# Optimization experiments

Hardware: AMD Instinct MI355X
Metric: run time of the kernel (lower is better)

The kernel has to match this reference:

```python
import jax, jax.numpy as jnp
import numpy as np
import math

B, DG, P, DA = 512, 1024, 1024, 256
LN_EPS = 1e-5  # torch LayerNorm default
EPS = 1e-12


def _ln(x, g, b):
    mu = jnp.mean(x, axis=-1, keepdims=True)
    var = jnp.mean((x - mu) ** 2, axis=-1, keepdims=True)
    return (x - mu) * jax.lax.rsqrt(var + LN_EPS) * g + b


def setup_inputs() -> dict:
    key = jax.random.key(0)
    ks = jax.random.split(key, 16)
    s = lambda fan_in: 1.0 / math.sqrt(fan_in)
    return {
        "hg": jax.random.normal(ks[0], (B, DG), jnp.float32),
        "desc_2d": jax.random.normal(ks[1], (B, P), jnp.float32),
        "Wq": jax.random.uniform(ks[2], (DA, DG), jnp.float32, -s(DG), s(DG)),
        "bq": jnp.zeros((DA,), jnp.float32),
        "wk_val": jax.random.uniform(ks[3], (DA,), jnp.float32, -1.0, 1.0),
        "bk_val": jax.random.uniform(ks[4], (DA,), jnp.float32, -1.0, 1.0),
        "wv_val": jax.random.uniform(ks[5], (DA,), jnp.float32, -1.0, 1.0),
        "bv_val": jax.random.uniform(ks[6], (DA,), jnp.float32, -1.0, 1.0),
        "Ek": jax.random.normal(ks[7], (P, DA), jnp.float32),
        "Ev": jax.random.normal(ks[8], (P, DA), jnp.float32),
        "Uq": jax.random.uniform(ks[9], (DA, DA), jnp.float32, -s(DA), s(DA)),
        "Vk": jax.random.uniform(ks[10], (DA, DA), jnp.float32, -s(DA), s(DA)),
        "ln_q_g": jnp.ones((DA,), jnp.float32), "ln_q_b": jnp.zeros((DA,), jnp.float32),
        "ln_k_g": jnp.ones((DA,), jnp.float32), "ln_k_b": jnp.zeros((DA,), jnp.float32),
        "ln_v_g": jnp.ones((DA,), jnp.float32), "ln_v_b": jnp.zeros((DA,), jnp.float32),
    }


def reference(hg, desc_2d, Wq, bq, wk_val, bk_val, wv_val, bv_val, Ek, Ev, Uq, Vk,
              ln_q_g, ln_q_b, ln_k_g, ln_k_b, ln_v_g, ln_v_b):
    # dropout is inference-mode (identity)
    q = _ln(hg @ Wq.T + bq, ln_q_g, ln_q_b)                       # (B, DA)
    # scalar -> token proj plus id embedding
    k = desc_2d[:, :, None] * wk_val + bk_val + Ek[None]          # (B, P, DA)
    v = desc_2d[:, :, None] * wv_val + bv_val + Ev[None]
    k = _ln(k, ln_k_g, ln_k_b)
    v = _ln(v, ln_v_g, ln_v_b)
    q2 = q @ Uq.T                                                 # (B, DA)
    k2 = jnp.einsum('bpd,ed->bpe', k, Vk)                         # (B, P, DA)
    e = jnp.einsum('bpd,bd->bp', k2, q2) / math.sqrt(DA)          # (B, P)
    alpha = jax.nn.sigmoid(e)
    alpha = alpha / (jnp.sum(alpha, axis=1, keepdims=True) + EPS)
    c = jnp.einsum('bp,bpd->bd', alpha, v)                        # (B, DA)
    return c, alpha
```

## Files before the change

### kernel.cpp

```cpp
#include <hip/hip_runtime.h>
#include <math.h>

#define B 512
#define DG 1024
#define P 1024
#define DA 256
#define LDP 68

__device__ __forceinline__ float block_reduce_sum(float v, volatile float* red) {
    #pragma unroll
    for (int off = 32; off > 0; off >>= 1) v += __shfl_down(v, off, 64);
    const int lane = threadIdx.x & 63, wid = threadIdx.x >> 6;
    __syncthreads();
    if (lane == 0) red[wid] = v;
    __syncthreads();
    return red[0] + red[1] + red[2] + red[3];
}

#define FMA16(a4, b4, acc)                                   \
    acc[0][0] = fmaf(a4.x, b4.x, acc[0][0]);                 \
    acc[0][1] = fmaf(a4.x, b4.y, acc[0][1]);                 \
    acc[0][2] = fmaf(a4.x, b4.z, acc[0][2]);                 \
    acc[0][3] = fmaf(a4.x, b4.w, acc[0][3]);                 \
    acc[1][0] = fmaf(a4.y, b4.x, acc[1][0]);                 \
    acc[1][1] = fmaf(a4.y, b4.y, acc[1][1]);                 \
    acc[1][2] = fmaf(a4.y, b4.z, acc[1][2]);                 \
    acc[1][3] = fmaf(a4.y, b4.w, acc[1][3]);                 \
    acc[2][0] = fmaf(a4.z, b4.x, acc[2][0]);                 \
    acc[2][1] = fmaf(a4.z, b4.y, acc[2][1]);                 \
    acc[2][2] = fmaf(a4.z, b4.z, acc[2][2]);                 \
    acc[2][3] = fmaf(a4.z, b4.w, acc[2][3]);                 \
    acc[3][0] = fmaf(a4.w, b4.x, acc[3][0]);                 \
    acc[3][1] = fmaf(a4.w, b4.y, acc[3][1]);                 \
    acc[3][2] = fmaf(a4.w, b4.z, acc[3][2]);                 \
    acc[3][3] = fmaf(a4.w, b4.w, acc[3][3]);

__global__ __launch_bounds__(256) void KA(const float* __restrict__ hg, const float* __restrict__ Wq,
                                          const float* __restrict__ Uq,
                                          const float* __restrict__ Ek, const float* __restrict__ Ev,
                                          const float* __restrict__ wk, const float* __restrict__ bk,
                                          const float* __restrict__ wv, const float* __restrict__ bv,
                                          float* __restrict__ qp, float* __restrict__ UqT,
                                          float* __restrict__ pst, float* __restrict__ scal4) {
    __shared__ __align__(16) float sA[32 * LDP];
    __shared__ __align__(16) float sB[32 * LDP];
    __shared__ float red[4];
    const int tid = threadIdx.x;
    const int bi = blockIdx.x;

    if (bi < 256) {
        const int mt = bi & 7, nt = (bi >> 3) & 3, ks = bi >> 5;
        const int b0 = mt * 64, d0 = nt * 64, kc = ks * 128;
        const int sm = tid >> 3, sk4 = (tid & 7) * 4;
        const int ty4 = (tid >> 4) * 4, tx4 = (tid & 15) * 4;
        float acc[4][4] = {};
        for (int kt = 0; kt < 128; kt += 32) {
            const int kg = kc + kt;
            #pragma unroll
            for (int pass = 0; pass < 2; ++pass) {
                int m = sm + pass * 32;
                float4 av = *reinterpret_cast<const float4*>(&hg[(b0 + m) * DG + kg + sk4]);
                sA[(sk4 + 0) * LDP + m] = av.x; sA[(sk4 + 1) * LDP + m] = av.y;
                sA[(sk4 + 2) * LDP + m] = av.z; sA[(sk4 + 3) * LDP + m] = av.w;
                float4 wv4 = *reinterpret_cast<const float4*>(&Wq[(d0 + m) * DG + kg + sk4]);
                sB[(sk4 + 0) * LDP + m] = wv4.x; sB[(sk4 + 1) * LDP + m] = wv4.y;
                sB[(sk4 + 2) * LDP + m] = wv4.z; sB[(sk4 + 3) * LDP + m] = wv4.w;
            }
            __syncthreads();
            #pragma unroll
            for (int kk = 0; kk < 32; ++kk) {
                float4 a4 = *reinterpret_cast<const float4*>(&sA[kk * LDP + ty4]);
                float4 b4 = *reinterpret_cast<const float4*>(&sB[kk * LDP + tx4]);
                FMA16(a4, b4, acc)
            }
            __syncthreads();
        }
        float* outp = qp + ks * (B * DA);
        #pragma unroll
        for (int i = 0; i < 4; ++i) {
            float4 o = make_float4(acc[i][0], acc[i][1], acc[i][2], acc[i][3]);
            *reinterpret_cast<float4*>(&outp[(b0 + ty4 + i) * DA + d0 + tx4]) = o;
        }
    } else if (bi < 320) {
        const int b2 = bi - 256;
        const int e0 = (b2 & 7) * 32, f0 = (b2 >> 3) * 32;
        const int col = tid & 31, row8 = tid >> 5;
        #pragma unroll
        for (int pass = 0; pass < 4; ++pass) {
            int r = row8 + pass * 8;
            sA[r * 33 + col] = Uq[(e0 + r) * DA + f0 + col];
        }
        __syncthreads();
        #pragma unroll
        for (int pass = 0; pass < 4; ++pass) {
            int r = row8 + pass * 8;
            UqT[(f0 + r) * DA + e0 + col] = sA[col * 33 + r];
        }
    } else {
        const int p = bi - 320, d = tid;
        const float inv = 1.0f / DA;
        float ek = Ek[p * DA + d], ev = Ev[p * DA + d];
        float wkd = wk[d], wvd = wv[d];
        float ck = bk[d] + ek, cv = bv[d] + ev;

        float Sck  = block_reduce_sum(ck, red);
        float Sck2 = block_reduce_sum(ck * ck, red);
        float Swck = block_reduce_sum(wkd * ck, red);
        float Scv  = block_reduce_sum(cv, red);
        float Scv2 = block_reduce_sum(cv * cv, red);
        float Swcv = block_reduce_sum(wvd * cv, red);
        float Swk  = block_reduce_sum(wkd, red);
        float Swv  = block_reduce_sum(wvd, red);

        float mwk = Swk * inv, mwv = Swv * inv;
        float mck = Sck * inv, mcv = Scv * inv;
        if (d == 0) {
            pst[0 * P + p] = mck;
            pst[1 * P + p] = Swck * inv - mwk * mck;
            pst[2 * P + p] = Sck2 * inv - mck * mck;
            pst[3 * P + p] = mcv;
            pst[4 * P + p] = Swcv * inv - mwv * mcv;
            pst[5 * P + p] = Scv2 * inv - mcv * mcv;
        }
        if (p == 0) {
            float Swk2 = block_reduce_sum(wkd * wkd, red);
            float Swv2 = block_reduce_sum(wvd * wvd, red);
            if (d == 0) {
                scal4[0] = mwk;
                scal4[1] = Swk2 * inv - mwk * mwk;
                scal4[2] = mwv;
                scal4[3] = Swv2 * inv - mwv * mwv;
            }
        }
    }
}

__global__ __launch_bounds__(256) void KC(const float* __restrict__ qp, const float* __restrict__ bq,
                                          const float* __restrict__ gq, const float* __restrict__ bqln,
                                          const float* __restrict__ UqT, const float* __restrict__ Vk,
                                          const float* __restrict__ gk,
                                          const float* __restrict__ wk, const float* __restrict__ bk,
                                          const float* __restrict__ bkln,
                                          float* __restrict__ gr, float* __restrict__ bscal) {
    __shared__ __align__(16) float q_lds[DA];
    __shared__ __align__(16) float q2_lds[DA];
    __shared__ float red[4];
    const int b = blockIdx.x, d = threadIdx.x;
    float x = bq[d];
    #pragma unroll
    for (int ks = 0; ks < 8; ++ks) x += qp[ks * (B * DA) + b * DA + d];
    float mu = block_reduce_sum(x, red) * (1.0f / DA);
    float xc = x - mu;
    float var = block_reduce_sum(xc * xc, red) * (1.0f / DA);
    float qv = xc * rsqrtf(var + 1e-5f) * gq[d] + bqln[d];
    q_lds[d] = qv;
    __syncthreads();

    float q2 = 0.f;
    for (int f = 0; f < DA; f += 4) {
        float4 qf = *reinterpret_cast<const float4*>(&q_lds[f]);
        q2 = fmaf(qf.x, UqT[(f + 0) * DA + d], q2);
        q2 = fmaf(qf.y, UqT[(f + 1) * DA + d], q2);
        q2 = fmaf(qf.z, UqT[(f + 2) * DA + d], q2);
        q2 = fmaf(qf.w, UqT[(f + 3) * DA + d], q2);
    }
    q2_lds[d] = q2;
    __syncthreads();

    float r = 0.f;
    for (int e = 0; e < DA; e += 4) {
        float4 qe = *reinterpret_cast<const float4*>(&q2_lds[e]);
        r = fmaf(qe.x, Vk[(e + 0) * DA + d], r);
        r = fmaf(qe.y, Vk[(e + 1) * DA + d], r);
        r = fmaf(qe.z, Vk[(e + 2) * DA + d], r);
        r = fmaf(qe.w, Vk[(e + 3) * DA + d], r);
    }
    float grv = gk[d] * r;
    gr[b * DA + d] = grv;

    float Wg = block_reduce_sum(wk[d] * grv, red);
    float Cg = block_reduce_sum(bk[d] * grv, red);
    float G  = block_reduce_sum(grv, red);
    float Bb = block_reduce_sum(bkln[d] * r, red);
    if (d == 0) {
        bscal[b] = Wg; bscal[B + b] = Cg; bscal[2 * B + b] = G; bscal[3 * B + b] = Bb;
    }
}

__global__ __launch_bounds__(256) void KD(const float* __restrict__ gr, const float* __restrict__ Ek,
                                          float* __restrict__ epart) {
    __shared__ __align__(16) float sA[32 * LDP];
    __shared__ __align__(16) float sB[32 * LDP];
    const int tid = threadIdx.x, bi = blockIdx.x;
    const int mt = bi & 7, nt = (bi >> 3) & 15, ks = bi >> 7;
    const int b0 = mt * 64, p0 = nt * 64, kc = ks * 128;
    const int sm = tid >> 3, sk4 = (tid & 7) * 4;
    const int ty4 = (tid >> 4) * 4, tx4 = (tid & 15) * 4;
    float acc[4][4] = {};
    for (int kt = 0; kt < 128; kt += 32) {
        const int kg = kc + kt;
        #pragma unroll
        for (int pass = 0; pass < 2; ++pass) {
            int m = sm + pass * 32;
            float4 av = *reinterpret_cast<const float4*>(&gr[(b0 + m) * DA + kg + sk4]);
            sA[(sk4 + 0) * LDP + m] = av.x; sA[(sk4 + 1) * LDP + m] = av.y;
            sA[(sk4 + 2) * LDP + m] = av.z; sA[(sk4 + 3) * LDP + m] = av.w;
            float4 ev = *reinterpret_cast<const float4*>(&Ek[(p0 + m) * DA + kg + sk4]);
            sB[(sk4 + 0) * LDP + m] = ev.x; sB[(sk4 + 1) * LDP + m] = ev.y;
            sB[(sk4 + 2) * LDP + m] = ev.z; sB[(sk4 + 3) * LDP + m] = ev.w;
        }
        __syncthreads();
        #pragma unroll
        for (int kk = 0; kk < 32; ++kk) {
            float4 a4 = *reinterpret_cast<const float4*>(&sA[kk * LDP + ty4]);
            float4 b4 = *reinterpret_cast<const float4*>(&sB[kk * LDP + tx4]);
            FMA16(a4, b4, acc)
        }
        __syncthreads();
    }
    float* outp = epart + ks * (B * P);
    #pragma unroll
    for (int i = 0; i < 4; ++i) {
        float4 o = make_float4(acc[i][0], acc[i][1], acc[i][2], acc[i][3]);
        *reinterpret_cast<float4*>(&outp[(b0 + ty4 + i) * P + p0 + tx4]) = o;
    }
}

__global__ __launch_bounds__(256) void KE(const float* __restrict__ epart, const float* __restrict__ desc,
                                          const float* __restrict__ bscal, const float* __restrict__ pst,
                                          const float* __restrict__ scal4,
                                          const float* __restrict__ gv, const float* __restrict__ wv,
                                          const float* __restrict__ bvv, const float* __restrict__ bvln,
                                          float* __restrict__ alpha_out, float* beta,
                                          float* __restrict__ out_c) {
    __shared__ float red[4];
    const int b = blockIdx.x, tid = threadIdx.x;
    const float mwk = scal4[0], Ak = scal4[1], mwv = scal4[2], Av = scal4[3];
    const float Wg = bscal[b], Cg = bscal[B + b], G = bscal[2 * B + b], Bb = bscal[3 * B + b];
    float u[4], sv[4];
    float usum = 0.f;
    #pragma unroll
    for (int j = 0; j < 4; ++j) {
        int p = j * 256 + tid;
        float dot = epart[b * P + p] + epart[B * P + b * P + p];
        float s = desc[b * P + p];
        float mck = pst[p], Bk = pst[P + p], Ck = pst[2 * P + p];
        float var = fmaf(s, fmaf(s, Ak, 2.0f * Bk), Ck);
        float rstd = rsqrtf(var + 1e-5f);
        float mu = fmaf(s, mwk, mck);
        float e = (rstd * (fmaf(s, Wg, Cg) + dot - mu * G) + Bb) * 0.0625f;
        float uu = 1.0f / (1.0f + expf(-e));
        u[j] = uu; sv[j] = s; usum += uu;
    }
    float S = block_reduce_sum(usum, red);
    float invS = 1.0f / (S + 1e-12f);
    float T = S * invS;
    float SB = 0.f, SBs = 0.f, SBm = 0.f;
    #pragma unroll
    for (int j = 0; j < 4; ++j) {
        int p = j * 256 + tid;
        float a = u[j] * invS;
        alpha_out[b * P + p] = a;
        float s = sv[j];
        float mcv = pst[3 * P + p], Bv = pst[4 * P + p], Cv = pst[5 * P + p];
        float var = fmaf(s, fmaf(s, Av, 2.0f * Bv), Cv);
        float rv = rsqrtf(var + 1e-5f);
        float bt = a * rv;
        beta[b * P + p] = bt;
        SB += bt;
        SBs = fmaf(bt, s, SBs);
        SBm = fmaf(bt, fmaf(s, mwv, mcv), SBm);
    }
    SB  = block_reduce_sum(SB, red);
    SBs = block_reduce_sum(SBs, red);
    SBm = block_reduce_sum(SBm, red);
    out_c[b * DA + tid] = gv[tid] * (wv[tid] * SBs + bvv[tid] * SB - SBm) + bvln[tid] * T;
}

__global__ __launch_bounds__(256) void KF(const float* __restrict__ beta, const float* __restrict__ Ev,
                                          float* __restrict__ cpart) {
    __shared__ __align__(16) float sA[32 * LDP];
    __shared__ __align__(16) float sB[32 * LDP];
    const int tid = threadIdx.x, bi = blockIdx.x;
    const int mt = bi & 7, nt = (bi >> 3) & 3, ks = bi >> 5;
    const int b0 = mt * 64, d0 = nt * 64, kc = ks * 128;
    const int sm = tid >> 3, sk4 = (tid & 7) * 4;
    const int kr = tid >> 4, n4 = (tid & 15) * 4;
    const int ty4 = (tid >> 4) * 4, tx4 = (tid & 15) * 4;
    float acc[4][4] = {};
    for (int kt = 0; kt < 128; kt += 32) {
        const int kg = kc + kt;
        #pragma unroll
        for (int pass = 0; pass < 2; ++pass) {
            int m = sm + pass * 32;
            float4 av = *reinterpret_cast<const float4*>(&beta[(b0 + m) * P + kg + sk4]);
            sA[(sk4 + 0) * LDP + m] = av.x; sA[(sk4 + 1) * LDP + m] = av.y;
            sA[(sk4 + 2) * LDP + m] = av.z; sA[(sk4 + 3) * LDP + m] = av.w;
            int k = kr + pass * 16;
            *reinterpret_cast<float4*>(&sB[k * LDP + n4]) =
                *reinterpret_cast<const float4*>(&Ev[(kg + k) * DA + d0 + n4]);
        }
        __syncthreads();
        #pragma unroll
        for (int kk = 0; kk < 32; ++kk) {
            float4 a4 = *reinterpret_cast<const float4*>(&sA[kk * LDP + ty4]);
            float4 b4 = *reinterpret_cast<const float4*>(&sB[kk * LDP + tx4]);
            FMA16(a4, b4, acc)
        }
        __syncthreads();
    }
    float* outp = cpart + ks * (B * DA);
    #pragma unroll
    for (int i = 0; i < 4; ++i) {
        float4 o = make_float4(acc[i][0], acc[i][1], acc[i][2], acc[i][3]);
        *reinterpret_cast<float4*>(&outp[(b0 + ty4 + i) * DA + d0 + tx4]) = o;
    }
}

__global__ __launch_bounds__(256) void KG(const float* __restrict__ cpart, const float* __restrict__ gv,
                                          float* __restrict__ out_c) {
    const int b = blockIdx.x, d = threadIdx.x;
    float s = 0.f;
    #pragma unroll
    for (int ks = 0; ks < 8; ++ks) s += cpart[ks * (B * DA) + b * DA + d];
    out_c[b * DA + d] = fmaf(gv[d], s, out_c[b * DA + d]);
}

extern "C" void kernel_launch(void* const* d_in, const int* in_sizes, int n_in,
                              void* d_out, int out_size, void* d_ws, size_t ws_size,
                              hipStream_t stream) {
    (void)in_sizes; (void)n_in; (void)out_size; (void)ws_size;
    const float* hg   = (const float*)d_in[0];
    const float* desc = (const float*)d_in[1];
    const float* Wq   = (const float*)d_in[2];
    const float* bq   = (const float*)d_in[3];
    const float* wk   = (const float*)d_in[4];
    const float* bk   = (const float*)d_in[5];
    const float* wv   = (const float*)d_in[6];
    const float* bv   = (const float*)d_in[7];
    const float* Ek   = (const float*)d_in[8];
    const float* Ev   = (const float*)d_in[9];
    const float* Uq   = (const float*)d_in[10];
    const float* Vk   = (const float*)d_in[11];
    const float* gq   = (const float*)d_in[12];
    const float* bqln = (const float*)d_in[13];
    const float* gk   = (const float*)d_in[14];
    const float* bkln = (const float*)d_in[15];
    const float* gv   = (const float*)d_in[16];
    const float* bvln = (const float*)d_in[17];

    float* out = (float*)d_out;
    float* out_c = out;
    float* out_alpha = out + B * DA;

    float* ws = (float*)d_ws;
    float* qp    = ws;
    float* epart = ws;
    float* beta  = ws;
    float* gr    = ws + 1048576;
    float* UqT   = ws + 1179648;
    float* cpart = ws + 524288;
    float* bscal = ws + 1572864;
    float* pst   = ws + 1574912;
    float* scal4 = ws + 1581056;

    KA<<<1344, 256, 0, stream>>>(hg, Wq, Uq, Ek, Ev, wk, bk, wv, bv, qp, UqT, pst, scal4);
    KC<<<512, 256, 0, stream>>>(qp, bq, gq, bqln, UqT, Vk, gk, wk, bk, bkln, gr, bscal);
    KD<<<256, 256, 0, stream>>>(gr, Ek, epart);
    KE<<<512, 256, 0, stream>>>(epart, desc, bscal, pst, scal4, gv, wv, bv, bvln, out_alpha, beta, out_c);
    KF<<<256, 256, 0, stream>>>(beta, Ev, cpart);
    KG<<<512, 256, 0, stream>>>(cpart, gv, out_c);
}
```

Measured before the change: 60.74 us.

## Reassociate attention scores via precomputed Uq^T Vk Ek matrix, defer normalization

Instead of computing q2 and gk*Vk^T q2 per batch row and then a B×P×DA GEMM against Ek, the code precomputes a batch-independent matrix N = Uq^T (gk∘Vk) Ek^T (DA×P) in KA/KC. Scores then come from a single q·N GEMM with K=DA that is fused with the sigmoid/LN-stat epilogue in KD, and the per-row scalar reductions come from precomputed vec4 vectors. Alpha normalization is deferred to the final kernel, so the Ev GEMM runs on unnormalized weights and KG rescales by 1/S. This drops one kernel launch and the split-K partials for the scores, but adds two DA×DA×P precompute GEMMs, more cpart splits and more workspace traffic.

After: 66.47 us. 9.4% more time.

```diff
diff --git a/kernel.cpp b/kernel.cpp
--- a/kernel.cpp
+++ b/kernel.cpp
@@ -35,13 +35,25 @@
     acc[3][2] = fmaf(a4.w, b4.z, acc[3][2]);                 \
     acc[3][3] = fmaf(a4.w, b4.w, acc[3][3]);
 
+#define FMA8(a0, a1, b4, acc)                                \
+    acc[0][0] = fmaf(a0, b4.x, acc[0][0]);                   \
+    acc[0][1] = fmaf(a0, b4.y, acc[0][1]);                   \
+    acc[0][2] = fmaf(a0, b4.z, acc[0][2]);                   \
+    acc[0][3] = fmaf(a0, b4.w, acc[0][3]);                   \
+    acc[1][0] = fmaf(a1, b4.x, acc[1][0]);                   \
+    acc[1][1] = fmaf(a1, b4.y, acc[1][1]);                   \
+    acc[1][2] = fmaf(a1, b4.z, acc[1][2]);                   \
+    acc[1][3] = fmaf(a1, b4.w, acc[1][3]);
+
 __global__ __launch_bounds__(256) void KA(const float* __restrict__ hg, const float* __restrict__ Wq,
-                                          const float* __restrict__ Uq,
+                                          const float* __restrict__ Uq, const float* __restrict__ Vk,
                                           const float* __restrict__ Ek, const float* __restrict__ Ev,
                                           const float* __restrict__ wk, const float* __restrict__ bk,
                                           const float* __restrict__ wv, const float* __restrict__ bv,
-                                          float* __restrict__ qp, float* __restrict__ UqT,
-                                          float* __restrict__ pst, float* __restrict__ scal4) {
+                                          const float* __restrict__ gk, const float* __restrict__ bkln,
+                                          float* __restrict__ qp, float* __restrict__ Gm,
+                                          float* __restrict__ pst, float* __restrict__ scal4,
+                                          float* __restrict__ vec4) {
     __shared__ __align__(16) float sA[32 * LDP];
     __shared__ __align__(16) float sB[32 * LDP];
     __shared__ float red[4];
@@ -81,23 +93,85 @@
             float4 o = make_float4(acc[i][0], acc[i][1], acc[i][2], acc[i][3]);
             *reinterpret_cast<float4*>(&outp[(b0 + ty4 + i) * DA + d0 + tx4]) = o;
         }
-    } else if (bi < 320) {
+    } else if (bi < 384) {
         const int b2 = bi - 256;
-        const int e0 = (b2 & 7) * 32, f0 = (b2 >> 3) * 32;
-        const int col = tid & 31, row8 = tid >> 5;
-        #pragma unroll
-        for (int pass = 0; pass < 4; ++pass) {
-            int r = row8 + pass * 8;
-            sA[r * 33 + col] = Uq[(e0 + r) * DA + f0 + col];
-        }
-        __syncthreads();
-        #pragma unroll
-        for (int pass = 0; pass < 4; ++pass) {
-            int r = row8 + pass * 8;
-            UqT[(f0 + r) * DA + e0 + col] = sA[col * 33 + r];
-        }
+        const int e0 = (b2 & 7) * 32, p0 = (b2 >> 3) * 64;
+        const int sm = tid >> 3, sk4 = (tid & 7) * 4;
+        const int ty = tid >> 4, tx4 = (tid & 15) * 4;
+        float acc[2][4] = {};
+        for (int kt = 0; kt < 256; kt += 32) {
+            float4 vv = *reinterpret_cast<const float4*>(&Vk[(e0 + sm) * DA + kt + sk4]);
+            float4 gg = *reinterpret_cast<const float4*>(&gk[kt + sk4]);
+            sA[(sk4 + 0) * LDP + sm] = vv.x * gg.x; sA[(sk4 + 1) * LDP + sm] = vv.y * gg.y;
+            sA[(sk4 + 2) * LDP + sm] = vv.z * gg.z; sA[(sk4 + 3) * LDP + sm] = vv.w * gg.w;
+            #pragma unroll
+            for (int pass = 0; pass < 2; ++pass) {
+                int m = sm + pass * 32;
+                float4 ee = *reinterpret_cast<const float4*>(&Ek[(p0 + m) * DA + kt + sk4]);
+                sB[(sk4 + 0) * LDP + m] = ee.x; sB[(sk4 + 1) * LDP + m] = ee.y;
+                sB[(sk4 + 2) * LDP + m] = ee.z; sB[(sk4 + 3) * LDP + m] = ee.w;
+            }
+            __syncthreads();
+            #pragma unroll
+            for (int kk = 0; kk < 32; ++kk) {
+                float a0 = sA[kk * LDP + ty * 2 + 0];
+                float a1 = sA[kk * LDP + ty * 2 + 1];
+                float4 b4 = *reinterpret_cast<const float4*>(&sB[kk * LDP + tx4]);
+                FMA8(a0, a1, b4, acc)
+            }
+            __syncthreads();
+        }
+        #pragma unroll
+        for (int i = 0; i < 2; ++i) {
+            float4 o = make_float4(acc[i][0], acc[i][1], acc[i][2], acc[i][3]);
+            *reinterpret_cast<float4*>(&Gm[(e0 + ty * 2 + i) * P + p0 + tx4]) = o;
+        }
+    } else if (bi == 384) {
+        float* w4  = sA;
+        float* tmp = sB;
+        float gkd = gk[tid];
+        w4[0 * 256 + tid] = wk[tid] * gkd;
+        w4[1 * 256 + tid] = bk[tid] * gkd;
+        w4[2 * 256 + tid] = gkd;
+        w4[3 * 256 + tid] = bkln[tid];
+        __syncthreads();
+        const int dl = tid & 15, eg = tid >> 4;
+        for (int eb = 0; eb < 16; ++eb) {
+            int e = eb * 16 + eg;
+            float p0 = 0.f, p1 = 0.f, p2 = 0.f, p3 = 0.f;
+            #pragma unroll
+            for (int t = 0; t < 16; ++t) {
+                int d = dl + t * 16;
+                float v = Vk[e * DA + d];
+                p0 = fmaf(v, w4[d], p0);
+                p1 = fmaf(v, w4[256 + d], p1);
+                p2 = fmaf(v, w4[512 + d], p2);
+                p3 = fmaf(v, w4[768 + d], p3);
+            }
+            #pragma unroll
+            for (int m = 8; m > 0; m >>= 1) {
+                p0 += __shfl_xor(p0, m, 16);
+                p1 += __shfl_xor(p1, m, 16);
+                p2 += __shfl_xor(p2, m, 16);
+                p3 += __shfl_xor(p3, m, 16);
+            }
+            if (dl == 0) {
+                tmp[e * 4 + 0] = p0; tmp[e * 4 + 1] = p1;
+                tmp[e * 4 + 2] = p2; tmp[e * 4 + 3] = p3;
+            }
+        }
+        __syncthreads();
+        float a0 = 0.f, a1 = 0.f, a2 = 0.f, a3 = 0.f;
+        for (int e = 0; e < 256; ++e) {
+            float u = Uq[e * DA + tid];
+            a0 = fmaf(u, tmp[e * 4 + 0], a0);
+            a1 = fmaf(u, tmp[e * 4 + 1], a1);
+            a2 = fmaf(u, tmp[e * 4 + 2], a2);
+            a3 = fmaf(u, tmp[e * 4 + 3], a3);
+        }
+        vec4[tid] = a0; vec4[256 + tid] = a1; vec4[512 + tid] = a2; vec4[768 + tid] = a3;
     } else {
-        const int p = bi - 320, d = tid;
+        const int p = bi - 385, d = tid;
         const float inv = 1.0f / DA;
         float ek = Ek[p * DA + d], ev = Ev[p * DA + d];
         float wkd = wk[d], wvd = wv[d];
@@ -137,163 +211,143 @@
 
 __global__ __launch_bounds__(256) void KC(const float* __restrict__ qp, const float* __restrict__ bq,
                                           const float* __restrict__ gq, const float* __restrict__ bqln,
-                                          const float* __restrict__ UqT, const float* __restrict__ Vk,
-                                          const float* __restrict__ gk,
-                                          const float* __restrict__ wk, const float* __restrict__ bk,
-                                          const float* __restrict__ bkln,
-                                          float* __restrict__ gr, float* __restrict__ bscal) {
-    __shared__ __align__(16) float q_lds[DA];
-    __shared__ __align__(16) float q2_lds[DA];
+                                          const float* __restrict__ vec4, const float* __restrict__ Uq,
+                                          const float* __restrict__ Gm,
+                                          float* __restrict__ qout, float* __restrict__ Nm,
+                                          float* __restrict__ bscal) {
+    __shared__ __align__(16) float sA[32 * LDP];
+    __shared__ __align__(16) float sB[32 * LDP];
     __shared__ float red[4];
-    const int b = blockIdx.x, d = threadIdx.x;
-    float x = bq[d];
-    #pragma unroll
-    for (int ks = 0; ks < 8; ++ks) x += qp[ks * (B * DA) + b * DA + d];
-    float mu = block_reduce_sum(x, red) * (1.0f / DA);
-    float xc = x - mu;
-    float var = block_reduce_sum(xc * xc, red) * (1.0f / DA);
-    float qv = xc * rsqrtf(var + 1e-5f) * gq[d] + bqln[d];
-    q_lds[d] = qv;
-    __syncthreads();
-
-    float q2 = 0.f;
-    for (int f = 0; f < DA; f += 4) {
-        float4 qf = *reinterpret_cast<const float4*>(&q_lds[f]);
-        q2 = fmaf(qf.x, UqT[(f + 0) * DA + d], q2);
-        q2 = fmaf(qf.y, UqT[(f + 1) * DA + d], q2);
-        q2 = fmaf(qf.z, UqT[(f + 2) * DA + d], q2);
-        q2 = fmaf(qf.w, UqT[(f + 3) * DA + d], q2);
-    }
-    q2_lds[d] = q2;
-    __syncthreads();
-
-    float r = 0.f;
-    for (int e = 0; e < DA; e += 4) {
-        float4 qe = *reinterpret_cast<const float4*>(&q2_lds[e]);
-        r = fmaf(qe.x, Vk[(e + 0) * DA + d], r);
-        r = fmaf(qe.y, Vk[(e + 1) * DA + d], r);
-        r = fmaf(qe.z, Vk[(e + 2) * DA + d], r);
-        r = fmaf(qe.w, Vk[(e + 3) * DA + d], r);
-    }
-    float grv = gk[d] * r;
-    gr[b * DA + d] = grv;
-
-    float Wg = block_reduce_sum(wk[d] * grv, red);
-    float Cg = block_reduce_sum(bk[d] * grv, red);
-    float G  = block_reduce_sum(grv, red);
-    float Bb = block_reduce_sum(bkln[d] * r, red);
-    if (d == 0) {
-        bscal[b] = Wg; bscal[B + b] = Cg; bscal[2 * B + b] = G; bscal[3 * B + b] = Bb;
-    }
-}
-
-__global__ __launch_bounds__(256) void KD(const float* __restrict__ gr, const float* __restrict__ Ek,
-                                          float* __restrict__ epart) {
+    const int tid = threadIdx.x;
+    const int bi = blockIdx.x;
+
+    if (bi < 512) {
+        const int b = bi, d = tid;
+        float x = bq[d];
+        #pragma unroll
+        for (int ks = 0; ks < 8; ++ks) x += qp[ks * (B * DA) + b * DA + d];
+        float mu = block_reduce_sum(x, red) * (1.0f / DA);
+        float xc = x - mu;
+        float var = block_reduce_sum(xc * xc, red) * (1.0f / DA);
+        float qv = xc * rsqrtf(var + 1e-5f) * gq[d] + bqln[d];
+        qout[b * DA + d] = qv;
+        float Wg = block_reduce_sum(qv * vec4[d], red);
+        float Cg = block_reduce_sum(qv * vec4[256 + d], red);
+        float G_ = block_reduce_sum(qv * vec4[512 + d], red);
+        float Bb = block_reduce_sum(qv * vec4[768 + d], red);
+        if (d == 0) {
+            bscal[b] = Wg; bscal[B + b] = Cg; bscal[2 * B + b] = G_; bscal[3 * B + b] = Bb;
+        }
+    } else {
+        const int b2 = bi - 512;
+        const int f0 = (b2 & 7) * 32, p0 = (b2 >> 3) * 64;
+        const int sm = tid >> 3, sk4 = (tid & 7) * 4;
+        const int kr = tid >> 4, n4 = (tid & 15) * 4;
+        const int ty = tid >> 4, tx4 = (tid & 15) * 4;
+        float acc[2][4] = {};
+        for (int kt = 0; kt < 256; kt += 32) {
+            *reinterpret_cast<float4*>(&sA[sm * LDP + sk4]) =
+                *reinterpret_cast<const float4*>(&Uq[(kt + sm) * DA + f0 + sk4]);
+            #pragma unroll
+            for (int pass = 0; pass < 2; ++pass) {
+                int k = kr + pass * 16;
+                *reinterpret_cast<float4*>(&sB[k * LDP + n4]) =
+                    *reinterpret_cast<const float4*>(&Gm[(kt + k) * P + p0 + n4]);
+            }
+            __syncthreads();
+            #pragma unroll
+            for (int kk = 0; kk < 32; ++kk) {
+                float a0 = sA[kk * LDP + ty * 2 + 0];
+                float a1 = sA[kk * LDP + ty * 2 + 1];
+                float4 b4 = *reinterpret_cast<const float4*>(&sB[kk * LDP + tx4]);
+                FMA8(a0, a1, b4, acc)
+            }
+            __syncthreads();
+        }
+        #pragma unroll
+        for (int i = 0; i < 2; ++i) {
+            float4 o = make_float4(acc[i][0], acc[i][1], acc[i][2], acc[i][3]);
+            *reinterpret_cast<float4*>(&Nm[(f0 + ty * 2 + i) * P + p0 + tx4]) = o;
+        }
+    }
+}
+
+__global__ __launch_bounds__(256) void KD(const float* __restrict__ q, const float* __restrict__ Nm,
+                                          const float* __restrict__ desc, const float* __restrict__ bscal,
+                                          const float* __restrict__ pst, const float* __restrict__ scal4,
+                                          float* __restrict__ u_out, float* __restrict__ w) {
     __shared__ __align__(16) float sA[32 * LDP];
     __shared__ __align__(16) float sB[32 * LDP];
     const int tid = threadIdx.x, bi = blockIdx.x;
-    const int mt = bi & 7, nt = (bi >> 3) & 15, ks = bi >> 7;
-    const int b0 = mt * 64, p0 = nt * 64, kc = ks * 128;
+    const int b0 = (bi & 15) * 32, p0 = (bi >> 4) * 64;
     const int sm = tid >> 3, sk4 = (tid & 7) * 4;
-    const int ty4 = (tid >> 4) * 4, tx4 = (tid & 15) * 4;
-    float acc[4][4] = {};
-    for (int kt = 0; kt < 128; kt += 32) {
-        const int kg = kc + kt;
+    const int kr = tid >> 4, n4 = (tid & 15) * 4;
+    const int ty = tid >> 4, tx4 = (tid & 15) * 4;
+    float acc[2][4] = {};
+    for (int kt = 0; kt < 256; kt += 32) {
+        float4 qv4 = *reinterpret_cast<const float4*>(&q[(b0 + sm) * DA + kt + sk4]);
+        sA[(sk4 + 0) * LDP + sm] = qv4.x; sA[(sk4 + 1) * LDP + sm] = qv4.y;
+        sA[(sk4 + 2) * LDP + sm] = qv4.z; sA[(sk4 + 3) * LDP + sm] = qv4.w;
         #pragma unroll
         for (int pass = 0; pass < 2; ++pass) {
-            int m = sm + pass * 32;
-            float4 av = *reinterpret_cast<const float4*>(&gr[(b0 + m) * DA + kg + sk4]);
-            sA[(sk4 + 0) * LDP + m] = av.x; sA[(sk4 + 1) * LDP + m] = av.y;
-            sA[(sk4 + 2) * LDP + m] = av.z; sA[(sk4 + 3) * LDP + m] = av.w;
-            float4 ev = *reinterpret_cast<const float4*>(&Ek[(p0 + m) * DA + kg + sk4]);
-            sB[(sk4 + 0) * LDP + m] = ev.x; sB[(sk4 + 1) * LDP + m] = ev.y;
-            sB[(sk4 + 2) * LDP + m] = ev.z; sB[(sk4 + 3) * LDP + m] = ev.w;
+            int k = kr + pass * 16;
+            *reinterpret_cast<float4*>(&sB[k * LDP + n4]) =
+                *reinterpret_cast<const float4*>(&Nm[(kt + k) * P + p0 + n4]);
         }
         __syncthreads();
         #pragma unroll
         for (int kk = 0; kk < 32; ++kk) {
-            float4 a4 = *reinterpret_cast<const float4*>(&sA[kk * LDP + ty4]);
+            float a0 = sA[kk * LDP + ty * 2 + 0];
+            float a1 = sA[kk * LDP + ty * 2 + 1];
             float4 b4 = *reinterpret_cast<const float4*>(&sB[kk * LDP + tx4]);
-            FMA16(a4, b4, acc)
-        }
-        __syncthreads();
-    }
-    float* outp = epart + ks * (B * P);
-    #pragma unroll
-    for (int i = 0; i < 4; ++i) {
-        float4 o = make_float4(acc[i][0], acc[i][1], acc[i][2], acc[i][3]);
-        *reinterpret_cast<float4*>(&outp[(b0 + ty4 + i) * P + p0 + tx4]) = o;
-    }
-}
-
-__global__ __launch_bounds__(256) void KE(const float* __restrict__ epart, const float* __restrict__ desc,
-                                          const float* __restrict__ bscal, const float* __restrict__ pst,
-                                          const float* __restrict__ scal4,
-                                          const float* __restrict__ gv, const float* __restrict__ wv,
-                                          const float* __restrict__ bvv, const float* __restrict__ bvln,
-                                          float* __restrict__ alpha_out, float* beta,
-                                          float* __restrict__ out_c) {
-    __shared__ float red[4];
-    const int b = blockIdx.x, tid = threadIdx.x;
-    const float mwk = scal4[0], Ak = scal4[1], mwv = scal4[2], Av = scal4[3];
-    const float Wg = bscal[b], Cg = bscal[B + b], G = bscal[2 * B + b], Bb = bscal[3 * B + b];
-    float u[4], sv[4];
-    float usum = 0.f;
-    #pragma unroll
-    for (int j = 0; j < 4; ++j) {
-        int p = j * 256 + tid;
-        float dot = epart[b * P + p] + epart[B * P + b * P + p];
-        float s = desc[b * P + p];
-        float mck = pst[p], Bk = pst[P + p], Ck = pst[2 * P + p];
-        float var = fmaf(s, fmaf(s, Ak, 2.0f * Bk), Ck);
-        float rstd = rsqrtf(var + 1e-5f);
-        float mu = fmaf(s, mwk, mck);
-        float e = (rstd * (fmaf(s, Wg, Cg) + dot - mu * G) + Bb) * 0.0625f;
-        float uu = 1.0f / (1.0f + expf(-e));
-        u[j] = uu; sv[j] = s; usum += uu;
-    }
-    float S = block_reduce_sum(usum, red);
-    float invS = 1.0f / (S + 1e-12f);
-    float T = S * invS;
-    float SB = 0.f, SBs = 0.f, SBm = 0.f;
-    #pragma unroll
-    for (int j = 0; j < 4; ++j) {
-        int p = j * 256 + tid;
-        float a = u[j] * invS;
-        alpha_out[b * P + p] = a;
-        float s = sv[j];
-        float mcv = pst[3 * P + p], Bv = pst[4 * P + p], Cv = pst[5 * P + p];
-        float var = fmaf(s, fmaf(s, Av, 2.0f * Bv), Cv);
-        float rv = rsqrtf(var + 1e-5f);
-        float bt = a * rv;
-        beta[b * P + p] = bt;
-        SB += bt;
-        SBs = fmaf(bt, s, SBs);
-        SBm = fmaf(bt, fmaf(s, mwv, mcv), SBm);
-    }
-    SB  = block_reduce_sum(SB, red);
-    SBs = block_reduce_sum(SBs, red);
-    SBm = block_reduce_sum(SBm, red);
-    out_c[b * DA + tid] = gv[tid] * (wv[tid] * SBs + bvv[tid] * SB - SBm) + bvln[tid] * T;
-}
-
-__global__ __launch_bounds__(256) void KF(const float* __restrict__ beta, const float* __restrict__ Ev,
+            FMA8(a0, a1, b4, acc)
+        }
+        __syncthreads();
+    }
+    const float mwk = scal4[0], Ak = scal4[1], Av = scal4[3];
+    #pragma unroll
+    for (int i = 0; i < 2; ++i) {
+        int b = b0 + ty * 2 + i;
+        float Wg = bscal[b], Cg = bscal[B + b], G_ = bscal[2 * B + b], Bb = bscal[3 * B + b];
+        float4 uo, wo;
+        float* up = &uo.x; float* wp = &wo.x;
+        #pragma unroll
+        for (int j = 0; j < 4; ++j) {
+            int p = p0 + tx4 + j;
+            float s = desc[b * P + p];
+            float mck = pst[p], Bk = pst[P + p], Ck = pst[2 * P + p];
+            float var = fmaf(s, fmaf(s, Ak, 2.0f * Bk), Ck);
+            float rstd = rsqrtf(var + 1e-5f);
+            float mu = fmaf(s, mwk, mck);
+            float e = (rstd * (fmaf(s, Wg, Cg) + acc[i][j] - mu * G_) + Bb) * 0.0625f;
+            float uu = 1.0f / (1.0f + expf(-e));
+            float Bv = pst[4 * P + p], Cv = pst[5 * P + p];
+            float varv = fmaf(s, fmaf(s, Av, 2.0f * Bv), Cv);
+            float rv = rsqrtf(varv + 1e-5f);
+            up[j] = uu; wp[j] = uu * rv;
+        }
+        *reinterpret_cast<float4*>(&u_out[b * P + p0 + tx4]) = uo;
+        *reinterpret_cast<float4*>(&w[b * P + p0 + tx4]) = wo;
+    }
+}
+
+__global__ __launch_bounds__(256) void KF(const float* __restrict__ w, const float* __restrict__ Ev,
                                           float* __restrict__ cpart) {
     __shared__ __align__(16) float sA[32 * LDP];
     __shared__ __align__(16) float sB[32 * LDP];
     const int tid = threadIdx.x, bi = blockIdx.x;
     const int mt = bi & 7, nt = (bi >> 3) & 3, ks = bi >> 5;
-    const int b0 = mt * 64, d0 = nt * 64, kc = ks * 128;
+    const int b0 = mt * 64, d0 = nt * 64, kc = ks * 64;
     const int sm = tid >> 3, sk4 = (tid & 7) * 4;
     const int kr = tid >> 4, n4 = (tid & 15) * 4;
     const int ty4 = (tid >> 4) * 4, tx4 = (tid & 15) * 4;
     float acc[4][4] = {};
-    for (int kt = 0; kt < 128; kt += 32) {
+    for (int kt = 0; kt < 64; kt += 32) {
         const int kg = kc + kt;
         #pragma unroll
         for (int pass = 0; pass < 2; ++pass) {
             int m = sm + pass * 32;
-            float4 av = *reinterpret_cast<const float4*>(&beta[(b0 + m) * P + kg + sk4]);
+            float4 av = *reinterpret_cast<const float4*>(&w[(b0 + m) * P + kg + sk4]);
             sA[(sk4 + 0) * LDP + m] = av.x; sA[(sk4 + 1) * LDP + m] = av.y;
             sA[(sk4 + 2) * LDP + m] = av.z; sA[(sk4 + 3) * LDP + m] = av.w;
             int k = kr + pass * 16;
@@ -317,13 +371,38 @@
     }
 }
 
-__global__ __launch_bounds__(256) void KG(const float* __restrict__ cpart, const float* __restrict__ gv,
+__global__ __launch_bounds__(256) void KG(const float* __restrict__ desc, const float* __restrict__ pst,
+                                          const float* __restrict__ scal4, const float* __restrict__ cpart,
+                                          const float* __restrict__ gv, const float* __restrict__ wv,
+                                          const float* __restrict__ bvv, const float* __restrict__ bvln,
+                                          float* __restrict__ alpha_io, const float* __restrict__ wbuf,
                                           float* __restrict__ out_c) {
-    const int b = blockIdx.x, d = threadIdx.x;
-    float s = 0.f;
-    #pragma unroll
-    for (int ks = 0; ks < 8; ++ks) s += cpart[ks * (B * DA) + b * DA + d];
-    out_c[b * DA + d] = fmaf(gv[d], s, out_c[b * DA + d]);
+    __shared__ float red[4];
+    const int b = blockIdx.x, tid = threadIdx.x;
+    const float mwv = scal4[2];
+    float u[4], wl[4], sv[4], mv[4];
+    #pragma unroll
+    for (int j = 0; j < 4; ++j) {
+        int p = j * 256 + tid;
+        u[j]  = alpha_io[b * P + p];
+        wl[j] = wbuf[b * P + p];
+        sv[j] = desc[b * P + p];
+        mv[j] = fmaf(sv[j], mwv, pst[3 * P + p]);
+    }
+    float S   = block_reduce_sum(u[0] + u[1] + u[2] + u[3], red);
+    float SB  = block_reduce_sum(wl[0] + wl[1] + wl[2] + wl[3], red);
+    float SBs = block_reduce_sum(wl[0]*sv[0] + wl[1]*sv[1] + wl[2]*sv[2] + wl[3]*sv[3], red);
+    float SBm = block_reduce_sum(wl[0]*mv[0] + wl[1]*mv[1] + wl[2]*mv[2] + wl[3]*mv[3], red);
+    float invS = 1.0f / (S + 1e-12f);
+    float T = S * invS;
+    #pragma unroll
+    for (int j = 0; j < 4; ++j)
+        alpha_io[b * P + j * 256 + tid] = u[j] * invS;
+    const int d = tid;
+    float csum = 0.f;
+    #pragma unroll
+    for (int ks = 0; ks < 16; ++ks) csum += cpart[ks * (B * DA) + b * DA + d];
+    out_c[b * DA + d] = invS * (gv[d] * (wv[d] * SBs + bvv[d] * SB + csum - SBm)) + bvln[d] * T;
 }
 
 extern "C" void kernel_launch(void* const* d_in, const int* in_sizes, int n_in,
@@ -355,19 +434,20 @@
 
     float* ws = (float*)d_ws;
     float* qp    = ws;
-    float* epart = ws;
-    float* beta  = ws;
-    float* gr    = ws + 1048576;
-    float* UqT   = ws + 1179648;
-    float* cpart = ws + 524288;
-    float* bscal = ws + 1572864;
-    float* pst   = ws + 1574912;
-    float* scal4 = ws + 1581056;
-
-    KA<<<1344, 256, 0, stream>>>(hg, Wq, Uq, Ek, Ev, wk, bk, wv, bv, qp, UqT, pst, scal4);
-    KC<<<512, 256, 0, stream>>>(qp, bq, gq, bqln, UqT, Vk, gk, wk, bk, bkln, gr, bscal);
-    KD<<<256, 256, 0, stream>>>(gr, Ek, epart);
-    KE<<<512, 256, 0, stream>>>(epart, desc, bscal, pst, scal4, gv, wv, bv, bvln, out_alpha, beta, out_c);
-    KF<<<256, 256, 0, stream>>>(beta, Ev, cpart);
-    KG<<<512, 256, 0, stream>>>(cpart, gv, out_c);
-}
+    float* Gm    = ws + 1048576;
+    float* Nm    = ws + 1310720;
+    float* q     = ws + 1572864;
+    float* w     = ws + 1703936;
+    float* cpart = ws + 2228224;
+    float* vec4  = ws + 4325376;
+    float* bscal = ws + 4326400;
+    float* pst   = ws + 4328448;
+    float* scal4 = ws + 4334592;
+
+    KA<<<1409, 256, 0, stream>>>(hg, Wq, Uq, Vk, Ek, Ev, wk, bk, wv, bv, gk, bkln,
+                                 qp, Gm, pst, scal4, vec4);
+    KC<<<640, 256, 0, stream>>>(qp, bq, gq, bqln, vec4, Uq, Gm, q, Nm, bscal);
+    KD<<<256, 256, 0, stream>>>(q, Nm, desc, bscal, pst, scal4, out_alpha, w);
+    KF<<<512, 256, 0, stream>>>(w, Ev, cpart);
+    KG<<<512, 256, 0, stream>>>(desc, pst, scal4, cpart, gv, wv, bv, bvln, out_alpha, w, out_c);
+}
```
